# Performance work log

Measured on AMD Instinct MI355X. Metric: run time of the kernel, lower is better.

Reference implementation:

```python
import jax, jax.numpy as jnp
import numpy as np

B, T, D = 4, 8192, 768
H, K, V = 12, 64, 64
EPS_RMS = 1e-6
EPS_NORM = 1e-12  # F.normalize default eps


def setup_inputs() -> dict:
    key = jax.random.key(0)
    ks = jax.random.split(key, 7)
    s = 1.0 / np.sqrt(D)
    return {
        "x": jax.random.normal(ks[0], (B, T, D), jnp.float32),
        "w_norm": jnp.ones((D,), jnp.float32),
        "Wk": jax.random.normal(ks[1], (D, H * K), jnp.float32) * s,   # stored [in,out]
        "Wv": jax.random.normal(ks[2], (D, H * V), jnp.float32) * s,
        "Wo": jax.random.normal(ks[3], (H * V, D), jnp.float32) * (1.0 / np.sqrt(H * V)),
        "Wb": jax.random.normal(ks[4], (D, H), jnp.float32) * s,
        "bb": jnp.full((H,), -2.0, jnp.float32),  # delta_beta_init
        "Wg": jax.random.normal(ks[5], (D, H), jnp.float32) * s,
        "bg": jnp.full((H,), 2.0, jnp.float32),   # delta_g_init
    }


def reference(x, w_norm, Wk, Wv, Wo, Wb, bb, Wg, bg):
    Bx, Tx, Dx = x.shape
    # RMSNorm
    xn = x * jax.lax.rsqrt(jnp.mean(x * x, axis=-1, keepdims=True) + EPS_RMS) * w_norm
    k = (xn @ Wk).reshape(Bx, Tx, H, K)
    v = (xn @ Wv).reshape(Bx, Tx, H, V)
    beta = jax.nn.sigmoid(xn @ Wb + bb)  # [B,T,H]
    g = jax.nn.sigmoid(xn @ Wg + bg)     # [B,T,H]
    # L2-normalize keys along head dim (F.normalize, p=2)
    k = k / jnp.maximum(jnp.linalg.norm(k, axis=-1, keepdims=True), EPS_NORM)

    def step(state, inp):
        # state: [B,H,K,V]
        k_t, v_t, b_t, g_t = inp  # [B,H,K],[B,H,V],[B,H],[B,H]
        pred = jnp.einsum('bhkv,bhk->bhv', state, k_t)
        err = v_t - pred
        state = g_t[..., None, None] * state + b_t[..., None, None] * (
            k_t[..., None] * err[:, :, None, :])
        out_t = jnp.einsum('bhkv,bhk->bhv', state, k_t)
        return state, out_t

    init = jnp.zeros((Bx, H, K, V), x.dtype)
    xs = (jnp.swapaxes(k, 0, 1), jnp.swapaxes(v, 0, 1),
          jnp.swapaxes(beta, 0, 1), jnp.swapaxes(g, 0, 1))
    final_state, outs = jax.lax.scan(step, init, xs)  # outs: [T,B,H,V]
    delta = jnp.swapaxes(outs, 0, 1).reshape(Bx, Tx, H * V) @ Wo
    out = x + delta
    return out, final_state
```

## Files before the change

kernel.cpp:

```cpp
#include <hip/hip_runtime.h>
#include <hip/hip_bf16.h>


typedef __attribute__((ext_vector_type(8))) short short8;
typedef __attribute__((ext_vector_type(4))) float floatx4;

#define DEVFN static __device__ __forceinline__

typedef const __attribute__((address_space(1))) unsigned int* as1_u32p;
typedef __attribute__((address_space(3))) unsigned int* as3_u32p;

DEVFN void gll16(const void* g, void* l) {
  __builtin_amdgcn_global_load_lds((as1_u32p)g, (as3_u32p)l, 16, 0, 0);
}

DEVFN unsigned short f2bf_u(float f) {
  __hip_bfloat16 h = __float2bfloat16(f);
  return __builtin_bit_cast(unsigned short, h);
}
DEVFN float bf2f(unsigned short u) {
  return __bfloat162float(__builtin_bit_cast(__hip_bfloat16, u));
}

static constexpr int T_LEN = 8192;
static constexpr int ROWS  = 4 * 8192;
static constexpr int D     = 768;
static constexpr int NKV   = 1664;
static constexpr int NC    = 128;
static constexpr int NBH   = 48;
static constexpr int NWG1  = NBH * NC;
static constexpr int NG    = 16;
static constexpr int NGRP  = NBH * NG;

DEVFN int swz16(int row, int slot) {
  return (row << 7) + (((slot ^ (row & 7)) & 7) << 4);
}
DEVFN int swzE(int row, int col) {
  return (row << 7) + ((((col >> 3) ^ (row & 7)) & 7) << 4) + ((col & 7) << 1);
}
DEVFN void st_bf(char* base, int row, int col, float v) {
  *(unsigned short*)(base + swzE(row, col)) = f2bf_u(v);
}
DEVFN float ld_bf(const char* base, int row, int col) {
  return bf2f(*(const unsigned short*)(base + swzE(row, col)));
}
DEVFN void mm16x64(const char* aB, const char* bB, int wv, int lane, floatx4 acc[4]) {
  #pragma unroll
  for (int ks = 0; ks < 2; ++ks) {
    short8 af = *(const short8*)(aB + swz16(wv * 16 + (lane & 15), ks * 4 + (lane >> 4)));
    #pragma unroll
    for (int t = 0; t < 4; ++t) {
      short8 bf = *(const short8*)(bB + swz16(t * 16 + (lane & 15), ks * 4 + (lane >> 4)));
      acc[t] = __builtin_amdgcn_mfma_f32_16x16x32_bf16(af, bf, acc[t], 0, 0, 0);
    }
  }
}

__global__ void k_prep_wt(const float* __restrict__ Wk, const float* __restrict__ Wv,
                          const float* __restrict__ Wb, const float* __restrict__ Wg,
                          __hip_bfloat16* __restrict__ WT) {
  int idx = blockIdx.x * 256 + threadIdx.x;
  if (idx >= NKV * D) return;
  int n = idx / D, k = idx % D;
  float v;
  if (n < 768)       v = Wk[k * 768 + n];
  else if (n < 1536) v = Wv[k * 768 + (n - 768)];
  else if (n < 1548) v = Wb[k * 12 + (n - 1536)];
  else if (n < 1560) v = Wg[k * 12 + (n - 1548)];
  else               v = 0.f;
  WT[idx] = __float2bfloat16(v);
}

__global__ void k_prep_wo(const float* __restrict__ Wo, __hip_bfloat16* __restrict__ WoT) {
  int idx = blockIdx.x * 256 + threadIdx.x;
  int n = idx / D, k = idx % D;
  WoT[idx] = __float2bfloat16(Wo[k * 768 + n]);
}

__global__ void k_rmsnorm(const float* __restrict__ x, const float* __restrict__ wn,
                          __hip_bfloat16* __restrict__ xn) {
  int wid  = (blockIdx.x << 2) + (threadIdx.x >> 6);
  int lane = threadIdx.x & 63;
  const float* xr = x + (size_t)wid * D;
  float4 a = *(const float4*)(xr + lane * 4);
  float4 b = *(const float4*)(xr + 256 + lane * 4);
  float4 c = *(const float4*)(xr + 512 + lane * 4);
  float ss = a.x*a.x + a.y*a.y + a.z*a.z + a.w*a.w
           + b.x*b.x + b.y*b.y + b.z*b.z + b.w*b.w
           + c.x*c.x + c.y*c.y + c.z*c.z + c.w*c.w;
  #pragma unroll
  for (int m = 1; m < 64; m <<= 1) ss += __shfl_xor(ss, m);
  float rs = rsqrtf(ss * (1.f / 768.f) + 1e-6f);
  float4 w0 = *(const float4*)(wn + lane * 4);
  float4 w1 = *(const float4*)(wn + 256 + lane * 4);
  float4 w2 = *(const float4*)(wn + 512 + lane * 4);
  unsigned short* xo = (unsigned short*)(xn + (size_t)wid * D);
  ushort4 u;
  u.x = f2bf_u(a.x*rs*w0.x); u.y = f2bf_u(a.y*rs*w0.y); u.z = f2bf_u(a.z*rs*w0.z); u.w = f2bf_u(a.w*rs*w0.w);
  *(ushort4*)(xo + lane * 4) = u;
  u.x = f2bf_u(b.x*rs*w1.x); u.y = f2bf_u(b.y*rs*w1.y); u.z = f2bf_u(b.z*rs*w1.z); u.w = f2bf_u(b.w*rs*w1.w);
  *(ushort4*)(xo + 256 + lane * 4) = u;
  u.x = f2bf_u(c.x*rs*w2.x); u.y = f2bf_u(c.y*rs*w2.y); u.z = f2bf_u(c.z*rs*w2.z); u.w = f2bf_u(c.w*rs*w2.w);
  *(ushort4*)(xo + 512 + lane * 4) = u;
}

template <int EPI>
__global__ __launch_bounds__(256)
void k_gemm(const __hip_bfloat16* __restrict__ A, const __hip_bfloat16* __restrict__ Bt,
            __hip_bfloat16* __restrict__ Ck, __hip_bfloat16* __restrict__ Cv,
            float* __restrict__ Cbg, float* __restrict__ C0, const float* __restrict__ Xadd) {
  __shared__ __align__(16) unsigned short As[2][128 * 64];
  __shared__ __align__(16) unsigned short Bs[2][128 * 64];
  const int K = 768, NKT = 12;
  int tid = threadIdx.x, lane = tid & 63, w = tid >> 6;
  int wr = w >> 1, wc = w & 1;
  int bx = blockIdx.x;
  bx = (bx & 7) * 32 + (bx >> 3);
  int m0 = bx * 128, n0 = blockIdx.y * 128;
  floatx4 zero = {0.f, 0.f, 0.f, 0.f};
  floatx4 acc[4][4];
  #pragma unroll
  for (int i = 0; i < 4; ++i)
    #pragma unroll
    for (int j = 0; j < 4; ++j) acc[i][j] = zero;

  auto stage = [&](int buf, int kt) {
    #pragma unroll
    for (int it = 0; it < 4; ++it) {
      int L = it * 256 + tid;
      int r = L >> 3, s = L & 7, sg = s ^ (r & 7);
      gll16(A  + (size_t)(m0 + r) * K + kt * 64 + sg * 8, &As[buf][L * 8]);
      gll16(Bt + (size_t)(n0 + r) * K + kt * 64 + sg * 8, &Bs[buf][L * 8]);
    }
  };

  stage(0, 0);
  __syncthreads();
  int buf = 0;
  for (int kt = 0; kt < NKT; ++kt) {
    if (kt + 1 < NKT) stage(buf ^ 1, kt + 1);
    __builtin_amdgcn_s_setprio(1);
    #pragma unroll
    for (int ks = 0; ks < 2; ++ks) {
      int c = ks * 4 + (lane >> 4);
      short8 af[4], bfr[4];
      #pragma unroll
      for (int i = 0; i < 4; ++i) {
        int ri = wr * 64 + i * 16 + (lane & 15);
        af[i] = *(const short8*)&As[buf][ri * 64 + ((c ^ (ri & 7)) << 3)];
      }
      #pragma unroll
      for (int j = 0; j < 4; ++j) {
        int rj = wc * 64 + j * 16 + (lane & 15);
        bfr[j] = *(const short8*)&Bs[buf][rj * 64 + ((c ^ (rj & 7)) << 3)];
      }
      #pragma unroll
      for (int i = 0; i < 4; ++i)
        #pragma unroll
        for (int j = 0; j < 4; ++j)
          acc[i][j] = __builtin_amdgcn_mfma_f32_16x16x32_bf16(af[i], bfr[j], acc[i][j], 0, 0, 0);
    }
    __builtin_amdgcn_s_setprio(0);
    __syncthreads();
    buf ^= 1;
  }

  if constexpr (EPI == 0) {
    if (n0 < 768) {
      #pragma unroll
      for (int i = 0; i < 4; ++i) {
        #pragma unroll
        for (int r = 0; r < 4; ++r) {
          float ss = 0.f;
          #pragma unroll
          for (int j = 0; j < 4; ++j) { float t = acc[i][j][r]; ss = fmaf(t, t, ss); }
          ss += __shfl_xor(ss, 1); ss += __shfl_xor(ss, 2);
          ss += __shfl_xor(ss, 4); ss += __shfl_xor(ss, 8);
          float sc = 1.f / fmaxf(sqrtf(ss), 1e-12f);
          int mm = m0 + wr * 64 + i * 16 + (lane >> 4) * 4 + r;
          #pragma unroll
          for (int j = 0; j < 4; ++j) {
            int n = n0 + wc * 64 + j * 16 + (lane & 15);
            Ck[(size_t)mm * 768 + n] = __float2bfloat16(acc[i][j][r] * sc);
          }
        }
      }
    } else if (n0 < 1536) {
      #pragma unroll
      for (int i = 0; i < 4; ++i)
        #pragma unroll
        for (int j = 0; j < 4; ++j) {
          int n = n0 + wc * 64 + j * 16 + (lane & 15) - 768;
          #pragma unroll
          for (int r = 0; r < 4; ++r) {
            int mm = m0 + wr * 64 + i * 16 + (lane >> 4) * 4 + r;
            Cv[(size_t)mm * 768 + n] = __float2bfloat16(acc[i][j][r]);
          }
        }
    } else {
      #pragma unroll
      for (int i = 0; i < 4; ++i)
        #pragma unroll
        for (int j = 0; j < 4; ++j) {
          int n = n0 + wc * 64 + j * 16 + (lane & 15) - 1536;
          #pragma unroll
          for (int r = 0; r < 4; ++r) {
            int mm = m0 + wr * 64 + i * 16 + (lane >> 4) * 4 + r;
            Cbg[(size_t)mm * 128 + n] = acc[i][j][r];
          }
        }
    }
  } else {
    #pragma unroll
    for (int i = 0; i < 4; ++i)
      #pragma unroll
      for (int j = 0; j < 4; ++j) {
        int n = n0 + wc * 64 + j * 16 + (lane & 15);
        #pragma unroll
        for (int r = 0; r < 4; ++r) {
          int mm = m0 + wr * 64 + i * 16 + (lane >> 4) * 4 + r;
          size_t o = (size_t)mm * 768 + n;
          C0[o] = Xadd[o] + acc[i][j][r];
        }
      }
  }
}

__global__ void k_betag(const float* __restrict__ bgraw, const float* __restrict__ bb,
                        const float* __restrict__ bgb, float* __restrict__ bgout) {
  int idx = blockIdx.x * 256 + threadIdx.x;
  if (idx >= ROWS * 24) return;
  int row = idx / 24, o = idx % 24;
  float bias = (o < 12) ? bb[o] : bgb[o - 12];
  float val = bgraw[(size_t)row * 128 + o] + bias;
  float s = 1.f / (1.f + __expf(-val));
  int col = (o < 12) ? (2 * o) : (2 * (o - 12) + 1);
  bgout[(size_t)row * 24 + col] = s;
}

__global__ void k_gates(const float* __restrict__ bgbuf, float* __restrict__ csbuf) {
  int wid  = blockIdx.x * 4 + (threadIdx.x >> 6);
  int lane = threadIdx.x & 63;
  int bh = wid >> 7, ck = wid & 127;
  int b = bh / 12, h = bh % 12;
  size_t row0 = (size_t)b * T_LEN + (size_t)ck * 64;
  float g = bgbuf[(row0 + lane) * 24 + h * 2 + 1];
  float lg = __log2f(g);
  float ci = lg;
  #pragma unroll
  for (int d = 1; d < 64; d <<= 1) { float t = __shfl_up(ci, d); if (lane >= d) ci += t; }
  csbuf[(size_t)wid * 128 + lane] = ci;
  csbuf[(size_t)wid * 128 + 64 + lane] = ci - lg;
}

__global__ __launch_bounds__(256)
void k_chunk1(const __hip_bfloat16* __restrict__ kb16, const __hip_bfloat16* __restrict__ vbuf,
              const float* __restrict__ bgbuf, const float* __restrict__ csbuf,
              __hip_bfloat16* __restrict__ Uvt_g, __hip_bfloat16* __restrict__ W_g) {
  __shared__ __align__(16) char sm[6 * 8192 + 768];
  char* SA = sm;
  char* SB = sm + 8192;
  char* SC = sm + 2 * 8192;
  char* SD = sm + 3 * 8192;
  char* SE = sm + 4 * 8192;
  char* SF = sm + 5 * 8192;
  float* cs   = (float*)(sm + 6 * 8192);
  float* cps  = (float*)(sm + 6 * 8192 + 256);
  float* bets = (float*)(sm + 6 * 8192 + 512);

  int blk = blockIdx.x, bh = blk >> 7, ck = blk & 127;
  int b = bh / 12, h = bh % 12;
  int tid = threadIdx.x, lane = tid & 63, wv = tid >> 6;
  size_t row0 = (size_t)b * T_LEN + (size_t)ck * 64;
  size_t wbase = (size_t)blk * 4096;

  if (tid < 64) {
    bets[tid] = bgbuf[(row0 + tid) * 24 + h * 2];
    cs[tid]   = csbuf[(size_t)blk * 128 + tid];
    cps[tid]  = csbuf[(size_t)blk * 128 + 64 + tid];
  }
  int sr = tid >> 2, sc0 = (tid & 3) * 16;
  {
    const __hip_bfloat16* kp = kb16 + (row0 + sr) * 768 + h * 64 + sc0;
    short8 k0 = *(const short8*)kp;
    short8 k1 = *(const short8*)(kp + 8);
    *(short8*)(SA + swz16(sr, sc0 >> 3)) = k0;
    *(short8*)(SA + swz16(sr, (sc0 >> 3) + 1)) = k1;
  }
  short8 vreg0, vreg1;
  {
    const __hip_bfloat16* vp = vbuf + (row0 + sr) * 768 + h * 64 + sc0;
    vreg0 = *(const short8*)vp;
    vreg1 = *(const short8*)(vp + 8);
  }
  __syncthreads();

  floatx4 acc[4];
  auto zacc = [&] {
    #pragma unroll
    for (int t = 0; t < 4; ++t) acc[t] = (floatx4){0.f, 0.f, 0.f, 0.f};
  };
  auto forRC = [&](auto&& f) {
    #pragma unroll
    for (int t = 0; t < 4; ++t)
      #pragma unroll
      for (int r = 0; r < 4; ++r)
        f(wv * 16 + (lane >> 4) * 4 + r, t * 16 + (lane & 15), acc[t][r]);
  };

  zacc(); mm16x64(SA, SA, wv, lane, acc);
  forRC([&](int i, int j, float v) {
    float Lv = 0.f;
    if (j < i) Lv = bets[i] * exp2f(cps[i] - cs[j]) * v;
    st_bf(SB, i, j, Lv);
    st_bf(SC, j, i, Lv);
    st_bf(SD, i, j, (i == j ? 1.f : 0.f) - Lv);
  });
  __syncthreads();

  auto power = [&](char* Ar, char* Bt, char* Or, char* Ot) {
    zacc(); mm16x64(Ar, Bt, wv, lane, acc);
    forRC([&](int i, int j, float v) { st_bf(Or, i, j, v); st_bf(Ot, j, i, v); });
    __syncthreads();
  };
  auto powerT = [&](char* Ar, char* Bt, char* Ot) {
    zacc(); mm16x64(Ar, Bt, wv, lane, acc);
    forRC([&](int i, int j, float v) { st_bf(Ot, j, i, v); });
    __syncthreads();
  };
  auto combine = [&](char* Mr, char* Pt, char* Out) {
    zacc(); mm16x64(Mr, Pt, wv, lane, acc);
    forRC([&](int i, int j, float v) { st_bf(Out, i, j, v + ld_bf(Mr, i, j)); });
    __syncthreads();
  };

  power(SB, SC, SE, SF);
  combine(SD, SF, SB);
  power(SE, SF, SC, SD);
  combine(SB, SD, SE);
  power(SC, SD, SF, SB);
  combine(SE, SB, SC);
  power(SF, SB, SD, SE);
  combine(SC, SE, SF);
  powerT(SD, SE, SB);
  combine(SF, SB, SC);

  {
    float be = bets[sr];
    #pragma unroll
    for (int q = 0; q < 8; ++q) {
      st_bf(SD, sc0 + q,     sr, be * bf2f(((unsigned short*)&vreg0)[q]));
      st_bf(SD, sc0 + 8 + q, sr, be * bf2f(((unsigned short*)&vreg1)[q]));
    }
    float scl = be * exp2f(cps[sr]);
    #pragma unroll
    for (int q = 0; q < 16; ++q) {
      float kv = ld_bf(SA, sr, sc0 + q);
      st_bf(SD, 64 + sc0 + q, sr, scl * kv);
    }
  }
  __syncthreads();

  {
    floatx4 xacc[8];
    #pragma unroll
    for (int t = 0; t < 8; ++t) xacc[t] = (floatx4){0.f, 0.f, 0.f, 0.f};
    #pragma unroll
    for (int ks = 0; ks < 2; ++ks) {
      short8 af = *(const short8*)(SC + swz16(wv * 16 + (lane & 15), ks * 4 + (lane >> 4)));
      #pragma unroll
      for (int t = 0; t < 8; ++t) {
        short8 bf = *(const short8*)(SD + swz16(t * 16 + (lane & 15), ks * 4 + (lane >> 4)));
        xacc[t] = __builtin_amdgcn_mfma_f32_16x16x32_bf16(af, bf, xacc[t], 0, 0, 0);
      }
    }
    #pragma unroll
    for (int t = 0; t < 8; ++t) {
      int c = t * 16 + (lane & 15);
      #pragma unroll
      for (int r = 0; r < 4; ++r) {
        int i = wv * 16 + (lane >> 4) * 4 + r;
        float v = xacc[t][r];
        if (c < 64) st_bf(SF, c, i, v);
        else        W_g[wbase + (size_t)(c - 64) * 64 + i] = __float2bfloat16(v);
      }
    }
  }
  __syncthreads();

  {
    int s2 = (tid & 3) * 2;
    short8 a0 = *(const short8*)(SF + swz16(sr, s2));
    short8 a1 = *(const short8*)(SF + swz16(sr, s2 + 1));
    *(short8*)(Uvt_g + wbase + (size_t)sr * 64 + s2 * 8) = a0;
    *(short8*)(Uvt_g + wbase + (size_t)sr * 64 + s2 * 8 + 8) = a1;
  }
}

__global__ __launch_bounds__(256)
void k_scanA(const __hip_bfloat16* __restrict__ kb16, const __hip_bfloat16* __restrict__ W_g,
             const __hip_bfloat16* __restrict__ Uvt_g, const float* __restrict__ csbuf,
             __hip_bfloat16* __restrict__ Ag_g, __hip_bfloat16* __restrict__ Bg_g) {
  __shared__ __align__(16) char sm[7 * 8192];
  char* SK  = sm;
  char* SW  = sm + 8192;
  char* SU  = sm + 2 * 8192;
  char* SAc = sm + 3 * 8192;
  char* SBc = sm + 4 * 8192;
  char* SAt = sm + 5 * 8192;
  char* SBa = sm + 6 * 8192;

  int blk = blockIdx.x, bh = blk >> 4, gg = blk & 15;
  int b = bh / 12, h = bh % 12;
  int tid = threadIdx.x, lane = tid & 63, wv = tid >> 6;
  int sr = tid >> 2, sc0 = (tid & 3) * 16, s2 = (tid & 3) * 2;
  int c0 = gg * 8;

  short8 z = {0, 0, 0, 0, 0, 0, 0, 0};
  *(short8*)(SAt + swz16(sr, s2)) = z;
  *(short8*)(SAt + swz16(sr, s2 + 1)) = z;
  *(short8*)(SBa + swz16(sr, s2)) = z;
  *(short8*)(SBa + swz16(sr, s2 + 1)) = z;
  __syncthreads();
  if (tid < 64) st_bf(SAt, tid, tid, 1.f);

  floatx4 acc[4];
  auto zacc = [&] {
    #pragma unroll
    for (int t = 0; t < 4; ++t) acc[t] = (floatx4){0.f, 0.f, 0.f, 0.f};
  };
  auto forRC = [&](auto&& f) {
    #pragma unroll
    for (int t = 0; t < 4; ++t)
      #pragma unroll
      for (int r = 0; r < 4; ++r)
        f(wv * 16 + (lane >> 4) * 4 + r, t * 16 + (lane & 15), acc[t][r]);
  };

  for (int cc = 0; cc < 8; ++cc) {
    int c = c0 + cc;
    size_t row0 = (size_t)b * T_LEN + (size_t)c * 64;
    size_t wb = ((size_t)bh * NC + c) * 4096;
    const float* csb = csbuf + (size_t)(bh * NC + c) * 128;
    float cs_sr = csb[sr], cs63 = csb[63];
    const __hip_bfloat16* kp = kb16 + (row0 + sr) * 768 + h * 64 + sc0;
    short8 k0 = *(const short8*)kp, k1 = *(const short8*)(kp + 8);
    const __hip_bfloat16* wp = W_g + wb + (size_t)sr * 64 + s2 * 8;
    short8 w0 = *(const short8*)wp, w1 = *(const short8*)(wp + 8);
    const __hip_bfloat16* up = Uvt_g + wb + (size_t)sr * 64 + s2 * 8;
    short8 u0 = *(const short8*)up, u1 = *(const short8*)(up + 8);
    float scl = exp2f(cs63 - cs_sr);
    #pragma unroll
    for (int q = 0; q < 8; ++q) {
      st_bf(SK, sc0 + q,     sr, scl * bf2f(((unsigned short*)&k0)[q]));
      st_bf(SK, sc0 + 8 + q, sr, scl * bf2f(((unsigned short*)&k1)[q]));
    }
    *(short8*)(SW + swz16(sr, s2)) = w0;
    *(short8*)(SW + swz16(sr, s2 + 1)) = w1;
    *(short8*)(SU + swz16(sr, s2)) = u0;
    *(short8*)(SU + swz16(sr, s2 + 1)) = u1;
    __syncthreads();
    float gC = exp2f(cs63);
    zacc(); mm16x64(SW, SK, wv, lane, acc);
    forRC([&](int i, int j, float v) { st_bf(SAc, j, i, ((i == j) ? gC : 0.f) - v); });
    zacc(); mm16x64(SU, SK, wv, lane, acc);
    forRC([&](int i, int j, float v) { st_bf(SBc, i, j, v); });
    __syncthreads();
    zacc(); mm16x64(SAt, SAc, wv, lane, acc);
    forRC([&](int i, int j, float v) { st_bf(SAt, i, j, v); });
    zacc(); mm16x64(SBa, SAc, wv, lane, acc);
    forRC([&](int i, int j, float v) { st_bf(SBa, i, j, v + ld_bf(SBc, i, j)); });
  }
  __syncthreads();
  size_t gb = (size_t)blk * 4096;
  #pragma unroll
  for (int q = 0; q < 16; ++q)
    Ag_g[gb + (size_t)(sc0 + q) * 64 + sr] = __float2bfloat16(ld_bf(SAt, sr, sc0 + q));
  {
    short8 b0 = *(const short8*)(SBa + swz16(sr, s2));
    short8 b1 = *(const short8*)(SBa + swz16(sr, s2 + 1));
    *(short8*)(Bg_g + gb + (size_t)sr * 64 + s2 * 8) = b0;
    *(short8*)(Bg_g + gb + (size_t)sr * 64 + s2 * 8 + 8) = b1;
  }
}

__global__ __launch_bounds__(256)
void k_scanB(const __hip_bfloat16* __restrict__ Ag_g, const __hip_bfloat16* __restrict__ Bg_g,
             __hip_bfloat16* __restrict__ Sg_g, float* __restrict__ fstate) {
  __shared__ __align__(16) char sm[3 * 8192];
  char* SSt = sm;
  char* SAg = sm + 8192;
  char* SBg = sm + 2 * 8192;
  int bh = blockIdx.x;
  int tid = threadIdx.x, lane = tid & 63, wv = tid >> 6;
  int sr = tid >> 2, s2 = (tid & 3) * 2;

  short8 z = {0, 0, 0, 0, 0, 0, 0, 0};
  *(short8*)(SSt + swz16(sr, s2)) = z;
  *(short8*)(SSt + swz16(sr, s2 + 1)) = z;

  floatx4 acc[4];
  for (int g = 0; g < NG; ++g) {
    size_t gb = ((size_t)bh * NG + g) * 4096;
    const __hip_bfloat16* pa = Ag_g + gb + (size_t)sr * 64 + s2 * 8;
    short8 a0 = *(const short8*)pa, a1 = *(const short8*)(pa + 8);
    const __hip_bfloat16* pb = Bg_g + gb + (size_t)sr * 64 + s2 * 8;
    short8 b0 = *(const short8*)pb, b1 = *(const short8*)(pb + 8);
    __syncthreads();
    {
      short8 s0 = *(const short8*)(SSt + swz16(sr, s2));
      short8 s1 = *(const short8*)(SSt + swz16(sr, s2 + 1));
      *(short8*)(Sg_g + gb + (size_t)sr * 64 + s2 * 8) = s0;
      *(short8*)(Sg_g + gb + (size_t)sr * 64 + s2 * 8 + 8) = s1;
    }
    *(short8*)(SAg + swz16(sr, s2)) = a0;
    *(short8*)(SAg + swz16(sr, s2 + 1)) = a1;
    *(short8*)(SBg + swz16(sr, s2)) = b0;
    *(short8*)(SBg + swz16(sr, s2 + 1)) = b1;
    __syncthreads();
    #pragma unroll
    for (int t = 0; t < 4; ++t) acc[t] = (floatx4){0.f, 0.f, 0.f, 0.f};
    mm16x64(SSt, SAg, wv, lane, acc);
    #pragma unroll
    for (int t = 0; t < 4; ++t) {
      int j = t * 16 + (lane & 15);
      #pragma unroll
      for (int r = 0; r < 4; ++r) {
        int i = wv * 16 + (lane >> 4) * 4 + r;
        float val = acc[t][r] + ld_bf(SBg, i, j);
        st_bf(SSt, i, j, val);
        if (g == NG - 1) fstate[(size_t)bh * 4096 + (size_t)j * 64 + i] = val;
      }
    }
  }
}

__global__ __launch_bounds__(256)
void k_scanC(const __hip_bfloat16* __restrict__ kb16, const __hip_bfloat16* __restrict__ W_g,
             __hip_bfloat16* __restrict__ Uvt_g, const float* __restrict__ csbuf,
             const __hip_bfloat16* __restrict__ Sg_g, __hip_bfloat16* __restrict__ Sst_g) {
  __shared__ __align__(16) char sm[7 * 8192];
  char* SK  = sm;
  char* SW  = sm + 8192;
  char* SW2 = sm + 2 * 8192;
  char* SU  = sm + 3 * 8192;
  char* SAc = sm + 4 * 8192;
  char* SBc = sm + 5 * 8192;
  char* SSt = sm + 6 * 8192;

  int blk = blockIdx.x, bh = blk >> 4, gg = blk & 15;
  int b = bh / 12, h = bh % 12;
  int tid = threadIdx.x, lane = tid & 63, wv = tid >> 6;
  int sr = tid >> 2, sc0 = (tid & 3) * 16, s2 = (tid & 3) * 2;
  int c0 = gg * 8;

  {
    const __hip_bfloat16* sp = Sg_g + (size_t)blk * 4096 + (size_t)sr * 64 + s2 * 8;
    short8 s0 = *(const short8*)sp, s1 = *(const short8*)(sp + 8);
    *(short8*)(SSt + swz16(sr, s2)) = s0;
    *(short8*)(SSt + swz16(sr, s2 + 1)) = s1;
  }

  floatx4 acc[4];
  auto zacc = [&] {
    #pragma unroll
    for (int t = 0; t < 4; ++t) acc[t] = (floatx4){0.f, 0.f, 0.f, 0.f};
  };
  auto forRC = [&](auto&& f) {
    #pragma unroll
    for (int t = 0; t < 4; ++t)
      #pragma unroll
      for (int r = 0; r < 4; ++r)
        f(wv * 16 + (lane >> 4) * 4 + r, t * 16 + (lane & 15), acc[t][r]);
  };

  for (int cc = 0; cc < 8; ++cc) {
    int c = c0 + cc;
    size_t row0 = (size_t)b * T_LEN + (size_t)c * 64;
    size_t wb = ((size_t)bh * NC + c) * 4096;
    const float* csb = csbuf + (size_t)(bh * NC + c) * 128;
    float cs_sr = csb[sr], cs63 = csb[63];
    const __hip_bfloat16* wp = W_g + wb + (size_t)sr * 64 + s2 * 8;
    short8 w0 = *(const short8*)wp, w1 = *(const short8*)(wp + 8);
    const __hip_bfloat16* up = Uvt_g + wb + (size_t)sr * 64 + s2 * 8;
    short8 u0 = *(const short8*)up, u1 = *(const short8*)(up + 8);
    short8 k0 = {0,0,0,0,0,0,0,0}, k1 = {0,0,0,0,0,0,0,0};
    if (cc < 7) {
      const __hip_bfloat16* kp = kb16 + (row0 + sr) * 768 + h * 64 + sc0;
      k0 = *(const short8*)kp; k1 = *(const short8*)(kp + 8);
    }
    __syncthreads();
    {
      short8 s0 = *(const short8*)(SSt + swz16(sr, s2));
      short8 s1 = *(const short8*)(SSt + swz16(sr, s2 + 1));
      *(short8*)(Sst_g + wb + (size_t)sr * 64 + s2 * 8) = s0;
      *(short8*)(Sst_g + wb + (size_t)sr * 64 + s2 * 8 + 8) = s1;
    }
    if (cc < 7) {
      float scl = exp2f(cs63 - cs_sr);
      #pragma unroll
      for (int q = 0; q < 8; ++q) {
        st_bf(SK, sc0 + q,     sr, scl * bf2f(((unsigned short*)&k0)[q]));
        st_bf(SK, sc0 + 8 + q, sr, scl * bf2f(((unsigned short*)&k1)[q]));
      }
      *(short8*)(SW + swz16(sr, s2)) = w0;
      *(short8*)(SW + swz16(sr, s2 + 1)) = w1;
    }
    #pragma unroll
    for (int q = 0; q < 8; ++q) {
      st_bf(SW2, sc0 + q,     sr, bf2f(((unsigned short*)&w0)[q]));
      st_bf(SW2, sc0 + 8 + q, sr, bf2f(((unsigned short*)&w1)[q]));
    }
    *(short8*)(SU + swz16(sr, s2)) = u0;
    *(short8*)(SU + swz16(sr, s2 + 1)) = u1;
    __syncthreads();
    zacc(); mm16x64(SSt, SW2, wv, lane, acc);
    forRC([&](int i, int j, float v) {
      Uvt_g[wb + (size_t)i * 64 + j] = __float2bfloat16(ld_bf(SU, i, j) - v);
    });
    if (cc == 7) break;
    float gC = exp2f(cs63);
    zacc(); mm16x64(SW, SK, wv, lane, acc);
    forRC([&](int i, int j, float v) { st_bf(SAc, j, i, ((i == j) ? gC : 0.f) - v); });
    zacc(); mm16x64(SU, SK, wv, lane, acc);
    forRC([&](int i, int j, float v) { st_bf(SBc, i, j, v); });
    __syncthreads();
    zacc(); mm16x64(SSt, SAc, wv, lane, acc);
    forRC([&](int i, int j, float v) { st_bf(SSt, i, j, v + ld_bf(SBc, i, j)); });
  }
}

__global__ __launch_bounds__(256)
void k_chunk3(const __hip_bfloat16* __restrict__ kb16, const float* __restrict__ csbuf,
              const __hip_bfloat16* __restrict__ Uvt_g, const __hip_bfloat16* __restrict__ Sst_g,
              __hip_bfloat16* __restrict__ outs) {
  __shared__ __align__(16) char sm[4 * 8192 + 256];
  char* SK = sm;
  char* SS = sm + 8192;
  char* SU = sm + 2 * 8192;
  char* SG = sm + 3 * 8192;
  float* cs = (float*)(sm + 4 * 8192);
  int blk = blockIdx.x, bh = blk >> 7, ck = blk & 127;
  int b = bh / 12, h = bh % 12;
  int tid = threadIdx.x, lane = tid & 63, wv = tid >> 6;
  size_t row0 = (size_t)b * T_LEN + (size_t)ck * 64;
  size_t wbase = (size_t)blk * 4096;
  int sr = tid >> 2, sc0 = (tid & 3) * 16;

  if (tid < 64) cs[tid] = csbuf[(size_t)blk * 128 + tid];
  {
    const __hip_bfloat16* kp = kb16 + (row0 + sr) * 768 + h * 64 + sc0;
    short8 a0 = *(const short8*)kp;
    short8 a1 = *(const short8*)(kp + 8);
    *(short8*)(SK + swz16(sr, sc0 >> 3)) = a0;
    *(short8*)(SK + swz16(sr, (sc0 >> 3) + 1)) = a1;
    const __hip_bfloat16* sp = Sst_g + wbase + (size_t)sr * 64 + sc0;
    a0 = *(const short8*)sp; a1 = *(const short8*)(sp + 8);
    *(short8*)(SS + swz16(sr, sc0 >> 3)) = a0;
    *(short8*)(SS + swz16(sr, (sc0 >> 3) + 1)) = a1;
    const __hip_bfloat16* up = Uvt_g + wbase + (size_t)sr * 64 + sc0;
    a0 = *(const short8*)up; a1 = *(const short8*)(up + 8);
    *(short8*)(SU + swz16(sr, sc0 >> 3)) = a0;
    *(short8*)(SU + swz16(sr, (sc0 >> 3) + 1)) = a1;
  }
  __syncthreads();

  floatx4 pAcc[4], acc[4];
  #pragma unroll
  for (int t = 0; t < 4; ++t) pAcc[t] = (floatx4){0.f, 0.f, 0.f, 0.f};
  mm16x64(SK, SS, wv, lane, pAcc);
  #pragma unroll
  for (int t = 0; t < 4; ++t) acc[t] = (floatx4){0.f, 0.f, 0.f, 0.f};
  mm16x64(SK, SK, wv, lane, acc);
  #pragma unroll
  for (int t = 0; t < 4; ++t) {
    int j = t * 16 + (lane & 15);
    float cj = cs[j];
    #pragma unroll
    for (int r = 0; r < 4; ++r) {
      int i = wv * 16 + (lane >> 4) * 4 + r;
      float gs = (j <= i) ? exp2f(cs[i] - cj) * acc[t][r] : 0.f;
      st_bf(SG, i, j, gs);
    }
  }
  __syncthreads();
  #pragma unroll
  for (int t = 0; t < 4; ++t) acc[t] = (floatx4){0.f, 0.f, 0.f, 0.f};
  mm16x64(SG, SU, wv, lane, acc);
  #pragma unroll
  for (int t = 0; t < 4; ++t) {
    int vc = t * 16 + (lane & 15);
    #pragma unroll
    for (int r = 0; r < 4; ++r) {
      int i = wv * 16 + (lane >> 4) * 4 + r;
      float o = exp2f(cs[i]) * pAcc[t][r] + acc[t][r];
      st_bf(SS, i, vc, o);
    }
  }
  __syncthreads();
  {
    int s2 = (tid & 3) * 2;
    short8 a0 = *(const short8*)(SS + swz16(sr, s2));
    short8 a1 = *(const short8*)(SS + swz16(sr, s2 + 1));
    __hip_bfloat16* op = outs + (row0 + sr) * 768 + h * 64 + s2 * 8;
    *(short8*)op = a0;
    *(short8*)(op + 8) = a1;
  }
}

extern "C" void kernel_launch(void* const* d_in, const int* in_sizes, int n_in,
                              void* d_out, int out_size, void* d_ws, size_t ws_size,
                              hipStream_t stream) {
  (void)in_sizes; (void)n_in; (void)out_size; (void)ws_size;
  const float* x   = (const float*)d_in[0];
  const float* wn  = (const float*)d_in[1];
  const float* Wk  = (const float*)d_in[2];
  const float* Wv  = (const float*)d_in[3];
  const float* Wo  = (const float*)d_in[4];
  const float* Wb  = (const float*)d_in[5];
  const float* bb  = (const float*)d_in[6];
  const float* Wg  = (const float*)d_in[7];
  const float* bgb = (const float*)d_in[8];
  float* out = (float*)d_out;

  char* ws = (char*)d_ws;
  size_t off = 0;
  const size_t TILE = (size_t)NWG1 * 4096 * 2;
  const size_t GTILE = (size_t)NGRP * 4096 * 2;
  __hip_bfloat16* xn   = (__hip_bfloat16*)(ws + off);
  __hip_bfloat16* Uvt  = (__hip_bfloat16*)(ws + off); off += TILE;
  __hip_bfloat16* WT   = (__hip_bfloat16*)(ws + off); off += (size_t)NKV * D * 2;
  __hip_bfloat16* WoT  = (__hip_bfloat16*)(ws + off); off += (size_t)D * D * 2;
  __hip_bfloat16* kb16 = (__hip_bfloat16*)(ws + off); off += (size_t)ROWS * D * 2;
  __hip_bfloat16* vbuf = (__hip_bfloat16*)(ws + off);
  __hip_bfloat16* Sst  = (__hip_bfloat16*)(ws + off); off += TILE;
  float* bgraw         = (float*)(ws + off);
  __hip_bfloat16* outsb= (__hip_bfloat16*)(ws + off);
  __hip_bfloat16* Ag_g = (__hip_bfloat16*)(ws + off);
  __hip_bfloat16* Bg_g = Ag_g + (size_t)NGRP * 4096;
  __hip_bfloat16* Sg_g = Bg_g + (size_t)NGRP * 4096;
  __hip_bfloat16* W_g  = Sg_g + (size_t)NGRP * 4096;
  off += 3 * GTILE + TILE;
  float* bgbuf         = (float*)(ws + off);          off += (size_t)ROWS * 24 * 4;
  float* csbuf         = (float*)(ws + off);          off += (size_t)NWG1 * 128 * 4;

  k_prep_wt<<<(NKV * D + 255) / 256, 256, 0, stream>>>(Wk, Wv, Wb, Wg, WT);
  k_prep_wo<<<(D * D) / 256, 256, 0, stream>>>(Wo, WoT);
  k_rmsnorm<<<ROWS / 4, 256, 0, stream>>>(x, wn, xn);
  k_gemm<0><<<dim3(ROWS / 128, NKV / 128), 256, 0, stream>>>(xn, WT, kb16, vbuf, bgraw, nullptr, nullptr);
  k_betag<<<(ROWS * 24) / 256, 256, 0, stream>>>(bgraw, bb, bgb, bgbuf);
  k_gates<<<NWG1 / 4, 256, 0, stream>>>(bgbuf, csbuf);
  k_chunk1<<<NWG1, 256, 0, stream>>>(kb16, vbuf, bgbuf, csbuf, Uvt, W_g);
  k_scanA<<<NGRP, 256, 0, stream>>>(kb16, W_g, Uvt, csbuf, Ag_g, Bg_g);
  k_scanB<<<NBH, 256, 0, stream>>>(Ag_g, Bg_g, Sg_g, out + (size_t)ROWS * D);
  k_scanC<<<NGRP, 256, 0, stream>>>(kb16, W_g, Uvt, csbuf, Sg_g, Sst);
  k_chunk3<<<NWG1, 256, 0, stream>>>(kb16, csbuf, Uvt, Sst, outsb);
  k_gemm<1><<<dim3(ROWS / 128, D / 128), 256, 0, stream>>>(outsb, WoT, nullptr, nullptr, nullptr, out, x);
}
```

Before: 529.1 us.

## Fuse scanC with chunk3, merge gate kernels, single-buffer GEMM LDS

Merges the beta/gate sigmoid kernel into the cumulative-log-gate kernel, which now writes beta into a widened per-chunk buffer, so the bgbuf intermediate goes away. Folds chunk3's intra-chunk output computation into the sequential scanC loop, so per-chunk states and corrected U no longer round-trip through global memory, and one launch is dropped. The GEMM also switches from double-buffered to single-buffered LDS staging with a sync after each load. That lowers LDS use but removes load/compute overlap, and the fused scan loop runs more serial work on only NGRP blocks instead of NWG1.

```diff
diff --git a/kernel.cpp b/kernel.cpp
--- a/kernel.cpp
+++ b/kernel.cpp
@@ -31,6 +31,7 @@
 static constexpr int NWG1  = NBH * NC;
 static constexpr int NG    = 16;
 static constexpr int NGRP  = NBH * NG;
+static constexpr int CSTR  = 192;
 
 DEVFN int swz16(int row, int slot) {
   return (row << 7) + (((slot ^ (row & 7)) & 7) << 4);
@@ -109,8 +110,8 @@
 void k_gemm(const __hip_bfloat16* __restrict__ A, const __hip_bfloat16* __restrict__ Bt,
             __hip_bfloat16* __restrict__ Ck, __hip_bfloat16* __restrict__ Cv,
             float* __restrict__ Cbg, float* __restrict__ C0, const float* __restrict__ Xadd) {
-  __shared__ __align__(16) unsigned short As[2][128 * 64];
-  __shared__ __align__(16) unsigned short Bs[2][128 * 64];
+  __shared__ __align__(16) unsigned short As[128 * 64];
+  __shared__ __align__(16) unsigned short Bs[128 * 64];
   const int K = 768, NKT = 12;
   int tid = threadIdx.x, lane = tid & 63, w = tid >> 6;
   int wr = w >> 1, wc = w & 1;
@@ -124,21 +125,19 @@
     #pragma unroll
     for (int j = 0; j < 4; ++j) acc[i][j] = zero;
 
-  auto stage = [&](int buf, int kt) {
+  auto stage = [&](int kt) {
     #pragma unroll
     for (int it = 0; it < 4; ++it) {
       int L = it * 256 + tid;
       int r = L >> 3, s = L & 7, sg = s ^ (r & 7);
-      gll16(A  + (size_t)(m0 + r) * K + kt * 64 + sg * 8, &As[buf][L * 8]);
-      gll16(Bt + (size_t)(n0 + r) * K + kt * 64 + sg * 8, &Bs[buf][L * 8]);
-    }
-  };
-
-  stage(0, 0);
-  __syncthreads();
-  int buf = 0;
+      gll16(A  + (size_t)(m0 + r) * K + kt * 64 + sg * 8, &As[L * 8]);
+      gll16(Bt + (size_t)(n0 + r) * K + kt * 64 + sg * 8, &Bs[L * 8]);
+    }
+  };
+
   for (int kt = 0; kt < NKT; ++kt) {
-    if (kt + 1 < NKT) stage(buf ^ 1, kt + 1);
+    stage(kt);
+    __syncthreads();
     __builtin_amdgcn_s_setprio(1);
     #pragma unroll
     for (int ks = 0; ks < 2; ++ks) {
@@ -147,12 +146,12 @@
       #pragma unroll
       for (int i = 0; i < 4; ++i) {
         int ri = wr * 64 + i * 16 + (lane & 15);
-        af[i] = *(const short8*)&As[buf][ri * 64 + ((c ^ (ri & 7)) << 3)];
+        af[i] = *(const short8*)&As[ri * 64 + ((c ^ (ri & 7)) << 3)];
       }
       #pragma unroll
       for (int j = 0; j < 4; ++j) {
         int rj = wc * 64 + j * 16 + (lane & 15);
-        bfr[j] = *(const short8*)&Bs[buf][rj * 64 + ((c ^ (rj & 7)) << 3)];
+        bfr[j] = *(const short8*)&Bs[rj * 64 + ((c ^ (rj & 7)) << 3)];
       }
       #pragma unroll
       for (int i = 0; i < 4; ++i)
@@ -162,7 +161,6 @@
     }
     __builtin_amdgcn_s_setprio(0);
     __syncthreads();
-    buf ^= 1;
   }
 
   if constexpr (EPI == 0) {
@@ -226,36 +224,28 @@
   }
 }
 
-__global__ void k_betag(const float* __restrict__ bgraw, const float* __restrict__ bb,
-                        const float* __restrict__ bgb, float* __restrict__ bgout) {
-  int idx = blockIdx.x * 256 + threadIdx.x;
-  if (idx >= ROWS * 24) return;
-  int row = idx / 24, o = idx % 24;
-  float bias = (o < 12) ? bb[o] : bgb[o - 12];
-  float val = bgraw[(size_t)row * 128 + o] + bias;
-  float s = 1.f / (1.f + __expf(-val));
-  int col = (o < 12) ? (2 * o) : (2 * (o - 12) + 1);
-  bgout[(size_t)row * 24 + col] = s;
-}
-
-__global__ void k_gates(const float* __restrict__ bgbuf, float* __restrict__ csbuf) {
+__global__ void k_gates2(const float* __restrict__ bgraw, const float* __restrict__ bb,
+                         const float* __restrict__ bgb, float* __restrict__ csbuf) {
   int wid  = blockIdx.x * 4 + (threadIdx.x >> 6);
   int lane = threadIdx.x & 63;
   int bh = wid >> 7, ck = wid & 127;
   int b = bh / 12, h = bh % 12;
   size_t row0 = (size_t)b * T_LEN + (size_t)ck * 64;
-  float g = bgbuf[(row0 + lane) * 24 + h * 2 + 1];
+  const float* br = bgraw + (row0 + lane) * 128;
+  float bet = 1.f / (1.f + __expf(-(br[h] + bb[h])));
+  float g   = 1.f / (1.f + __expf(-(br[12 + h] + bgb[h])));
   float lg = __log2f(g);
   float ci = lg;
   #pragma unroll
   for (int d = 1; d < 64; d <<= 1) { float t = __shfl_up(ci, d); if (lane >= d) ci += t; }
-  csbuf[(size_t)wid * 128 + lane] = ci;
-  csbuf[(size_t)wid * 128 + 64 + lane] = ci - lg;
+  csbuf[(size_t)wid * CSTR + lane] = ci;
+  csbuf[(size_t)wid * CSTR + 64 + lane] = ci - lg;
+  csbuf[(size_t)wid * CSTR + 128 + lane] = bet;
 }
 
 __global__ __launch_bounds__(256)
 void k_chunk1(const __hip_bfloat16* __restrict__ kb16, const __hip_bfloat16* __restrict__ vbuf,
-              const float* __restrict__ bgbuf, const float* __restrict__ csbuf,
+              const float* __restrict__ csbuf,
               __hip_bfloat16* __restrict__ Uvt_g, __hip_bfloat16* __restrict__ W_g) {
   __shared__ __align__(16) char sm[6 * 8192 + 768];
   char* SA = sm;
@@ -275,9 +265,9 @@
   size_t wbase = (size_t)blk * 4096;
 
   if (tid < 64) {
-    bets[tid] = bgbuf[(row0 + tid) * 24 + h * 2];
-    cs[tid]   = csbuf[(size_t)blk * 128 + tid];
-    cps[tid]  = csbuf[(size_t)blk * 128 + 64 + tid];
+    cs[tid]   = csbuf[(size_t)blk * CSTR + tid];
+    cps[tid]  = csbuf[(size_t)blk * CSTR + 64 + tid];
+    bets[tid] = csbuf[(size_t)blk * CSTR + 128 + tid];
   }
   int sr = tid >> 2, sc0 = (tid & 3) * 16;
   {
@@ -441,7 +431,7 @@
     int c = c0 + cc;
     size_t row0 = (size_t)b * T_LEN + (size_t)c * 64;
     size_t wb = ((size_t)bh * NC + c) * 4096;
-    const float* csb = csbuf + (size_t)(bh * NC + c) * 128;
+    const float* csb = csbuf + (size_t)(bh * NC + c) * CSTR;
     float cs_sr = csb[sr], cs63 = csb[63];
     const __hip_bfloat16* kp = kb16 + (row0 + sr) * 768 + h * 64 + sc0;
     short8 k0 = *(const short8*)kp, k1 = *(const short8*)(kp + 8);
@@ -536,23 +526,24 @@
 }
 
 __global__ __launch_bounds__(256)
-void k_scanC(const __hip_bfloat16* __restrict__ kb16, const __hip_bfloat16* __restrict__ W_g,
-             __hip_bfloat16* __restrict__ Uvt_g, const float* __restrict__ csbuf,
-             const __hip_bfloat16* __restrict__ Sg_g, __hip_bfloat16* __restrict__ Sst_g) {
+void k_scfuse(const __hip_bfloat16* __restrict__ kb16, const __hip_bfloat16* __restrict__ W_g,
+              const __hip_bfloat16* __restrict__ Uvt_g, const float* __restrict__ csbuf,
+              const __hip_bfloat16* __restrict__ Sg_g, __hip_bfloat16* __restrict__ outs) {
   __shared__ __align__(16) char sm[7 * 8192];
-  char* SK  = sm;
-  char* SW  = sm + 8192;
-  char* SW2 = sm + 2 * 8192;
-  char* SU  = sm + 3 * 8192;
-  char* SAc = sm + 4 * 8192;
-  char* SBc = sm + 5 * 8192;
-  char* SSt = sm + 6 * 8192;
+  char* SSt = sm;
+  char* SKr = sm + 8192;
+  char* SKt = sm + 2 * 8192;
+  char* SW  = sm + 3 * 8192;
+  char* SU  = sm + 4 * 8192;
+  char* SAc = sm + 5 * 8192;
+  char* SBc = sm + 6 * 8192;
 
   int blk = blockIdx.x, bh = blk >> 4, gg = blk & 15;
   int b = bh / 12, h = bh % 12;
   int tid = threadIdx.x, lane = tid & 63, wv = tid >> 6;
   int sr = tid >> 2, sc0 = (tid & 3) * 16, s2 = (tid & 3) * 2;
   int c0 = gg * 8;
+  int iR0 = wv * 16 + (lane >> 4) * 4;
 
   {
     const __hip_bfloat16* sp = Sg_g + (size_t)blk * 4096 + (size_t)sr * 64 + s2 * 8;
@@ -561,7 +552,7 @@
     *(short8*)(SSt + swz16(sr, s2 + 1)) = s1;
   }
 
-  floatx4 acc[4];
+  floatx4 acc[4], pAcc[4];
   auto zacc = [&] {
     #pragma unroll
     for (int t = 0; t < 4; ++t) acc[t] = (floatx4){0.f, 0.f, 0.f, 0.f};
@@ -571,140 +562,92 @@
     for (int t = 0; t < 4; ++t)
       #pragma unroll
       for (int r = 0; r < 4; ++r)
-        f(wv * 16 + (lane >> 4) * 4 + r, t * 16 + (lane & 15), acc[t][r]);
+        f(iR0 + r, t * 16 + (lane & 15), acc[t][r]);
   };
 
   for (int cc = 0; cc < 8; ++cc) {
     int c = c0 + cc;
     size_t row0 = (size_t)b * T_LEN + (size_t)c * 64;
     size_t wb = ((size_t)bh * NC + c) * 4096;
-    const float* csb = csbuf + (size_t)(bh * NC + c) * 128;
+    const float* csb = csbuf + (size_t)(bh * NC + c) * CSTR;
     float cs_sr = csb[sr], cs63 = csb[63];
-    const __hip_bfloat16* wp = W_g + wb + (size_t)sr * 64 + s2 * 8;
+    float csI[4], csJ[4];
+    #pragma unroll
+    for (int r = 0; r < 4; ++r) csI[r] = csb[iR0 + r];
+    #pragma unroll
+    for (int t = 0; t < 4; ++t) csJ[t] = csb[t * 16 + (lane & 15)];
+    const __hip_bfloat16* kp = kb16 + (row0 + sr) * 768 + h * 64 + sc0;
+    short8 k0 = *(const short8*)kp, k1 = *(const short8*)(kp + 8);
+    const __hip_bfloat16* wp = W_g + wb + (size_t)sr * 64 + sc0;
     short8 w0 = *(const short8*)wp, w1 = *(const short8*)(wp + 8);
-    const __hip_bfloat16* up = Uvt_g + wb + (size_t)sr * 64 + s2 * 8;
+    const __hip_bfloat16* up = Uvt_g + wb + (size_t)sr * 64 + sc0;
     short8 u0 = *(const short8*)up, u1 = *(const short8*)(up + 8);
-    short8 k0 = {0,0,0,0,0,0,0,0}, k1 = {0,0,0,0,0,0,0,0};
-    if (cc < 7) {
-      const __hip_bfloat16* kp = kb16 + (row0 + sr) * 768 + h * 64 + sc0;
-      k0 = *(const short8*)kp; k1 = *(const short8*)(kp + 8);
-    }
-    __syncthreads();
+    __syncthreads();
+    *(short8*)(SKr + swz16(sr, sc0 >> 3)) = k0;
+    *(short8*)(SKr + swz16(sr, (sc0 >> 3) + 1)) = k1;
     {
-      short8 s0 = *(const short8*)(SSt + swz16(sr, s2));
-      short8 s1 = *(const short8*)(SSt + swz16(sr, s2 + 1));
-      *(short8*)(Sst_g + wb + (size_t)sr * 64 + s2 * 8) = s0;
-      *(short8*)(Sst_g + wb + (size_t)sr * 64 + s2 * 8 + 8) = s1;
-    }
-    if (cc < 7) {
       float scl = exp2f(cs63 - cs_sr);
       #pragma unroll
       for (int q = 0; q < 8; ++q) {
-        st_bf(SK, sc0 + q,     sr, scl * bf2f(((unsigned short*)&k0)[q]));
-        st_bf(SK, sc0 + 8 + q, sr, scl * bf2f(((unsigned short*)&k1)[q]));
-      }
-      *(short8*)(SW + swz16(sr, s2)) = w0;
-      *(short8*)(SW + swz16(sr, s2 + 1)) = w1;
-    }
-    #pragma unroll
-    for (int q = 0; q < 8; ++q) {
-      st_bf(SW2, sc0 + q,     sr, bf2f(((unsigned short*)&w0)[q]));
-      st_bf(SW2, sc0 + 8 + q, sr, bf2f(((unsigned short*)&w1)[q]));
-    }
+        st_bf(SKt, sc0 + q,     sr, scl * bf2f(((unsigned short*)&k0)[q]));
+        st_bf(SKt, sc0 + 8 + q, sr, scl * bf2f(((unsigned short*)&k1)[q]));
+      }
+    }
+    *(short8*)(SW + swz16(sr, s2)) = w0;
+    *(short8*)(SW + swz16(sr, s2 + 1)) = w1;
     *(short8*)(SU + swz16(sr, s2)) = u0;
     *(short8*)(SU + swz16(sr, s2 + 1)) = u1;
     __syncthreads();
-    zacc(); mm16x64(SSt, SW2, wv, lane, acc);
-    forRC([&](int i, int j, float v) {
-      Uvt_g[wb + (size_t)i * 64 + j] = __float2bfloat16(ld_bf(SU, i, j) - v);
-    });
-    if (cc == 7) break;
     float gC = exp2f(cs63);
-    zacc(); mm16x64(SW, SK, wv, lane, acc);
+    zacc(); mm16x64(SW, SKt, wv, lane, acc);
     forRC([&](int i, int j, float v) { st_bf(SAc, j, i, ((i == j) ? gC : 0.f) - v); });
-    zacc(); mm16x64(SU, SK, wv, lane, acc);
+    zacc(); mm16x64(SU, SKt, wv, lane, acc);
     forRC([&](int i, int j, float v) { st_bf(SBc, i, j, v); });
     __syncthreads();
+    #pragma unroll
+    for (int q = 0; q < 8; ++q) {
+      st_bf(SW, sc0 + q,     sr, bf2f(((unsigned short*)&w0)[q]));
+      st_bf(SW, sc0 + 8 + q, sr, bf2f(((unsigned short*)&w1)[q]));
+    }
+    zacc(); mm16x64(SKr, SKr, wv, lane, acc);
+    #pragma unroll
+    for (int t = 0; t < 4; ++t) {
+      int j = t * 16 + (lane & 15);
+      #pragma unroll
+      for (int r = 0; r < 4; ++r) {
+        int i = iR0 + r;
+        float gs = (j <= i) ? exp2f(csI[r] - csJ[t]) * acc[t][r] : 0.f;
+        st_bf(SKt, i, j, gs);
+      }
+    }
+    __syncthreads();
+    #pragma unroll
+    for (int t = 0; t < 4; ++t) pAcc[t] = (floatx4){0.f, 0.f, 0.f, 0.f};
+    mm16x64(SKr, SSt, wv, lane, pAcc);
+    zacc(); mm16x64(SSt, SW, wv, lane, acc);
+    forRC([&](int i, int j, float v) { st_bf(SU, i, j, ld_bf(SU, i, j) - v); });
+    __syncthreads();
+    zacc(); mm16x64(SKt, SU, wv, lane, acc);
+    #pragma unroll
+    for (int t = 0; t < 4; ++t) {
+      int vc = t * 16 + (lane & 15);
+      #pragma unroll
+      for (int r = 0; r < 4; ++r) {
+        int i = iR0 + r;
+        float o = exp2f(csI[r]) * pAcc[t][r] + acc[t][r];
+        st_bf(SKr, i, vc, o);
+      }
+    }
     zacc(); mm16x64(SSt, SAc, wv, lane, acc);
     forRC([&](int i, int j, float v) { st_bf(SSt, i, j, v + ld_bf(SBc, i, j)); });
-  }
-}
-
-__global__ __launch_bounds__(256)
-void k_chunk3(const __hip_bfloat16* __restrict__ kb16, const float* __restrict__ csbuf,
-              const __hip_bfloat16* __restrict__ Uvt_g, const __hip_bfloat16* __restrict__ Sst_g,
-              __hip_bfloat16* __restrict__ outs) {
-  __shared__ __align__(16) char sm[4 * 8192 + 256];
-  char* SK = sm;
-  char* SS = sm + 8192;
-  char* SU = sm + 2 * 8192;
-  char* SG = sm + 3 * 8192;
-  float* cs = (float*)(sm + 4 * 8192);
-  int blk = blockIdx.x, bh = blk >> 7, ck = blk & 127;
-  int b = bh / 12, h = bh % 12;
-  int tid = threadIdx.x, lane = tid & 63, wv = tid >> 6;
-  size_t row0 = (size_t)b * T_LEN + (size_t)ck * 64;
-  size_t wbase = (size_t)blk * 4096;
-  int sr = tid >> 2, sc0 = (tid & 3) * 16;
-
-  if (tid < 64) cs[tid] = csbuf[(size_t)blk * 128 + tid];
-  {
-    const __hip_bfloat16* kp = kb16 + (row0 + sr) * 768 + h * 64 + sc0;
-    short8 a0 = *(const short8*)kp;
-    short8 a1 = *(const short8*)(kp + 8);
-    *(short8*)(SK + swz16(sr, sc0 >> 3)) = a0;
-    *(short8*)(SK + swz16(sr, (sc0 >> 3) + 1)) = a1;
-    const __hip_bfloat16* sp = Sst_g + wbase + (size_t)sr * 64 + sc0;
-    a0 = *(const short8*)sp; a1 = *(const short8*)(sp + 8);
-    *(short8*)(SS + swz16(sr, sc0 >> 3)) = a0;
-    *(short8*)(SS + swz16(sr, (sc0 >> 3) + 1)) = a1;
-    const __hip_bfloat16* up = Uvt_g + wbase + (size_t)sr * 64 + sc0;
-    a0 = *(const short8*)up; a1 = *(const short8*)(up + 8);
-    *(short8*)(SU + swz16(sr, sc0 >> 3)) = a0;
-    *(short8*)(SU + swz16(sr, (sc0 >> 3) + 1)) = a1;
-  }
-  __syncthreads();
-
-  floatx4 pAcc[4], acc[4];
-  #pragma unroll
-  for (int t = 0; t < 4; ++t) pAcc[t] = (floatx4){0.f, 0.f, 0.f, 0.f};
-  mm16x64(SK, SS, wv, lane, pAcc);
-  #pragma unroll
-  for (int t = 0; t < 4; ++t) acc[t] = (floatx4){0.f, 0.f, 0.f, 0.f};
-  mm16x64(SK, SK, wv, lane, acc);
-  #pragma unroll
-  for (int t = 0; t < 4; ++t) {
-    int j = t * 16 + (lane & 15);
-    float cj = cs[j];
-    #pragma unroll
-    for (int r = 0; r < 4; ++r) {
-      int i = wv * 16 + (lane >> 4) * 4 + r;
-      float gs = (j <= i) ? exp2f(cs[i] - cj) * acc[t][r] : 0.f;
-      st_bf(SG, i, j, gs);
-    }
-  }
-  __syncthreads();
-  #pragma unroll
-  for (int t = 0; t < 4; ++t) acc[t] = (floatx4){0.f, 0.f, 0.f, 0.f};
-  mm16x64(SG, SU, wv, lane, acc);
-  #pragma unroll
-  for (int t = 0; t < 4; ++t) {
-    int vc = t * 16 + (lane & 15);
-    #pragma unroll
-    for (int r = 0; r < 4; ++r) {
-      int i = wv * 16 + (lane >> 4) * 4 + r;
-      float o = exp2f(cs[i]) * pAcc[t][r] + acc[t][r];
-      st_bf(SS, i, vc, o);
-    }
-  }
-  __syncthreads();
-  {
-    int s2 = (tid & 3) * 2;
-    short8 a0 = *(const short8*)(SS + swz16(sr, s2));
-    short8 a1 = *(const short8*)(SS + swz16(sr, s2 + 1));
-    __hip_bfloat16* op = outs + (row0 + sr) * 768 + h * 64 + s2 * 8;
-    *(short8*)op = a0;
-    *(short8*)(op + 8) = a1;
+    __syncthreads();
+    {
+      short8 a0 = *(const short8*)(SKr + swz16(sr, s2));
+      short8 a1 = *(const short8*)(SKr + swz16(sr, s2 + 1));
+      __hip_bfloat16* op = outs + (row0 + sr) * 768 + h * 64 + s2 * 8;
+      *(short8*)op = a0;
+      *(short8*)(op + 8) = a1;
+    }
   }
 }
 
@@ -733,27 +676,23 @@
   __hip_bfloat16* WoT  = (__hip_bfloat16*)(ws + off); off += (size_t)D * D * 2;
   __hip_bfloat16* kb16 = (__hip_bfloat16*)(ws + off); off += (size_t)ROWS * D * 2;
   __hip_bfloat16* vbuf = (__hip_bfloat16*)(ws + off);
-  __hip_bfloat16* Sst  = (__hip_bfloat16*)(ws + off); off += TILE;
+  __hip_bfloat16* outsb= (__hip_bfloat16*)(ws + off); off += TILE;
   float* bgraw         = (float*)(ws + off);
-  __hip_bfloat16* outsb= (__hip_bfloat16*)(ws + off);
   __hip_bfloat16* Ag_g = (__hip_bfloat16*)(ws + off);
   __hip_bfloat16* Bg_g = Ag_g + (size_t)NGRP * 4096;
   __hip_bfloat16* Sg_g = Bg_g + (size_t)NGRP * 4096;
   __hip_bfloat16* W_g  = Sg_g + (size_t)NGRP * 4096;
   off += 3 * GTILE + TILE;
-  float* bgbuf         = (float*)(ws + off);          off += (size_t)ROWS * 24 * 4;
-  float* csbuf         = (float*)(ws + off);          off += (size_t)NWG1 * 128 * 4;
+  float* csbuf         = (float*)(ws + off);          off += (size_t)NWG1 * CSTR * 4;
 
   k_prep_wt<<<(NKV * D + 255) / 256, 256, 0, stream>>>(Wk, Wv, Wb, Wg, WT);
   k_prep_wo<<<(D * D) / 256, 256, 0, stream>>>(Wo, WoT);
   k_rmsnorm<<<ROWS / 4, 256, 0, stream>>>(x, wn, xn);
   k_gemm<0><<<dim3(ROWS / 128, NKV / 128), 256, 0, stream>>>(xn, WT, kb16, vbuf, bgraw, nullptr, nullptr);
-  k_betag<<<(ROWS * 24) / 256, 256, 0, stream>>>(bgraw, bb, bgb, bgbuf);
-  k_gates<<<NWG1 / 4, 256, 0, stream>>>(bgbuf, csbuf);
-  k_chunk1<<<NWG1, 256, 0, stream>>>(kb16, vbuf, bgbuf, csbuf, Uvt, W_g);
+  k_gates2<<<NWG1 / 4, 256, 0, stream>>>(bgraw, bb, bgb, csbuf);
+  k_chunk1<<<NWG1, 256, 0, stream>>>(kb16, vbuf, csbuf, Uvt, W_g);
   k_scanA<<<NGRP, 256, 0, stream>>>(kb16, W_g, Uvt, csbuf, Ag_g, Bg_g);
   k_scanB<<<NBH, 256, 0, stream>>>(Ag_g, Bg_g, Sg_g, out + (size_t)ROWS * D);
-  k_scanC<<<NGRP, 256, 0, stream>>>(kb16, W_g, Uvt, csbuf, Sg_g, Sst);
-  k_chunk3<<<NWG1, 256, 0, stream>>>(kb16, csbuf, Uvt, Sst, outsb);
+  k_scfuse<<<NGRP, 256, 0, stream>>>(kb16, W_g, Uvt, csbuf, Sg_g, outsb);
   k_gemm<1><<<dim3(ROWS / 128, D / 128), 256, 0, stream>>>(outsb, WoT, nullptr, nullptr, nullptr, out, x);
 }
```

Measured after the change: 543.6 us. 1.03x slower.
